# Kernel optimization log

Measured on AMD Instinct MI355X. Metric: run time of the kernel, lower is better.

The kernel has to match this reference:

```python
import math
import jax, jax.numpy as jnp
import numpy as np

TWO_PI = 2.0 * math.pi
LN_EPS = 1e-5


def wrap_angle(a):
    # wrap to (-pi, pi]
    return (a + math.pi) % TWO_PI - math.pi


def setup_inputs() -> dict:
    key = jax.random.key(0)
    ks = jax.random.split(key, 8)
    N = 2000          # num sources / targets (agents)
    E = 200000        # num edges
    D = 4             # input_dim (fixed by RelativeContextPositionEmbedding)
    NF = 64           # num_freq_bands
    H = 128           # hidden_dim
    F = 2 * NF + 1    # fourier feature width per input channel
    source = jax.random.normal(ks[0], (N, 3), jnp.float32)
    target = jax.random.normal(ks[1], (N, 5), jnp.float32)
    edge = jax.random.randint(ks[2], (2, E), 0, N, dtype=jnp.int32)
    freqs = jax.random.normal(ks[3], (D, NF), jnp.float32)          # nn.Embedding(D, NF).weight
    W1 = jax.random.normal(ks[4], (D, F, H), jnp.float32) * 0.02    # per-branch Linear1
    b1 = jnp.zeros((D, H), jnp.float32)
    gamma = jnp.ones((D, H), jnp.float32)                            # per-branch LayerNorm
    beta = jnp.zeros((D, H), jnp.float32)
    W2 = jax.random.normal(ks[5], (D, H, H), jnp.float32) * 0.02    # per-branch Linear2
    b2 = jnp.zeros((D, H), jnp.float32)
    return {"source": source, "target": target, "edge": edge, "freqs": freqs,
            "W1": W1, "b1": b1, "gamma": gamma, "beta": beta, "W2": W2, "b2": b2}


def _compute_feature(source, target, edge):
    src_pos, src_head = source[:, :2], source[:, 2]
    tgt_pos, tgt_head, tgt_speed = target[:, :2], target[:, 2], target[:, 3]
    e0, e1 = edge[0], edge[1]
    pd = src_pos[e0] - tgt_pos[e1]              # [E, 2]
    dx, dy = pd[:, 0], pd[:, 1]
    dh = wrap_angle(src_head[e0] - tgt_head[e1])
    ang = jnp.arctan2(dy, dx)
    tvx = tgt_speed * jnp.cos(tgt_head)
    tvy = tgt_speed * jnp.sin(tgt_head)
    closing = tvx[e1] * jnp.cos(ang) + tvy[e1] * jnp.sin(ang)
    return jnp.stack([dx, dy, dh, closing], axis=-1)  # [E, 4]


def reference(source, target, edge, freqs, W1, b1, gamma, beta, W2, b2):
    # feature computed under torch.no_grad() -> stop_gradient
    feat = jax.lax.stop_gradient(_compute_feature(source, target, edge))  # [E, D]
    x = feat[:, :, None] * freqs[None] * TWO_PI                            # [E, D, NF]
    x = jnp.concatenate([jnp.cos(x), jnp.sin(x), feat[:, :, None]], axis=-1)  # [E, D, F]
    # 4 small Linear -> LayerNorm -> ReLU -> Linear branches, vectorized over D
    h = jnp.einsum('edf,dfh->edh', x, W1) + b1                             # [E, D, H]
    mu = jnp.mean(h, axis=-1, keepdims=True)
    var = jnp.mean(jnp.square(h - mu), axis=-1, keepdims=True)
    h = (h - mu) * jax.lax.rsqrt(var + LN_EPS) * gamma + beta
    h = jax.nn.relu(h)
    y = jnp.einsum('edh,dhk->edk', h, W2) + b2                             # [E, D, H]
    return y.sum(axis=1)                                                   # [E, H]
```

## Files before the change

### kernel.cpp

```cpp
#include <hip/hip_runtime.h>
#include <hip/hip_bf16.h>
#include <math.h>

namespace {

typedef __attribute__((ext_vector_type(8))) short  short8;
typedef __attribute__((ext_vector_type(4))) float  float4v;

constexpr float PI_F     = 3.14159265358979323846f;
constexpr float TWO_PI_F = 6.28318530717958647692f;

__device__ __forceinline__ unsigned pack2(float a, float b) {
    __hip_bfloat162 h = __float22bfloat162_rn(float2{a, b});
    unsigned r;
    __builtin_memcpy(&r, &h, 4);
    return r;
}

union Frag { unsigned u[4]; short8 s; };

__device__ __forceinline__ void gl2lds16(const void* g, void* l) {
    __builtin_amdgcn_global_load_lds(
        (const __attribute__((address_space(1))) void*)g,
        (__attribute__((address_space(3))) void*)l, 16, 0, 0);
}

__device__ __forceinline__ void pb2() {
    asm volatile("s_waitcnt vmcnt(2) lgkmcnt(0)" ::: "memory");
    __builtin_amdgcn_s_barrier();
    __builtin_amdgcn_sched_barrier(0);
}
__device__ __forceinline__ void pb0() {
    asm volatile("s_waitcnt vmcnt(0) lgkmcnt(0)" ::: "memory");
    __builtin_amdgcn_s_barrier();
    __builtin_amdgcn_sched_barrier(0);
}

__global__ __launch_bounds__(256)
void prep_weights(const float* __restrict__ W1,
                  const float* __restrict__ W2,
                  ushort* __restrict__ W1T,
                  ushort* __restrict__ W2T) {
    const int idx = blockIdx.x * 256 + threadIdx.x;
    if (idx < 65536) {
        const int d = idx >> 14;
        const int n = (idx >> 7) & 127;
        const int k = idx & 127;
        __hip_bfloat16 v = __float2bfloat16(W1[(d * 129 + k) * 128 + n]);
        ushort u; __builtin_memcpy(&u, &v, 2);
        W1T[idx] = u;
    } else {
        const int j = idx - 65536;
        const int d = j >> 14;
        const int n = (j >> 7) & 127;
        const int kslot = j & 127;
        const int c = 32 * (kslot >> 5) + 16 * ((kslot >> 2) & 1)
                    + 4 * ((kslot >> 3) & 3) + (kslot & 3);
        __hip_bfloat16 v = __float2bfloat16(W2[(d * 128 + c) * 128 + n]);
        ushort u; __builtin_memcpy(&u, &v, 2);
        W2T[j] = u;
    }
}

__device__ __forceinline__ void stage_half(const ushort* __restrict__ Wtile,
                                           int half, ushort* slot, int wv, int lane) {
    const int e4 = lane & 15;
    const int g  = lane >> 4;
    #pragma unroll
    for (int i = 0; i < 2; ++i) {
        const int c  = 2 * wv + i;
        const int tt = c >> 2;
        const int ks = c & 3;
        const ushort* gp = Wtile + (16 * (4 * half + tt) + e4) * 128 + g * 8 + 32 * ks;
        gl2lds16(gp, slot + c * 512);
    }
}

__global__ __launch_bounds__(512, 4)
void rcpe_rot(const float* __restrict__ source,
              const float* __restrict__ target,
              const int*   __restrict__ edge,
              const float* __restrict__ freqs,
              const float* __restrict__ W1,
              const ushort* __restrict__ W1T,
              const float* __restrict__ b1,
              const float* __restrict__ gamma,
              const float* __restrict__ beta,
              const ushort* __restrict__ W2T,
              const float* __restrict__ b2,
              float* __restrict__ out,
              int E)
{
    __shared__ __align__(16) ushort wbuf[3][8192];
    __shared__ __align__(16) float b1_lds[4][128];
    __shared__ __align__(16) float gm_lds[4][128];
    __shared__ __align__(16) float bt_lds[4][128];
    __shared__ __align__(16) float w1r_lds[4][128];
    __shared__ __align__(16) float feat_lds[4][128];
    __shared__ __align__(16) float freq_lds[4][64];

    const int tid  = threadIdx.x;
    const int wv   = tid >> 6;
    const int lane = tid & 63;
    const int e4   = lane & 15;
    const int g    = lane >> 4;
    const int ebase = blockIdx.x * 128;
    const int eg    = ebase + wv * 16 + e4;

    stage_half(W1T, 0, wbuf[0], wv, lane);
    stage_half(W1T, 1, wbuf[1], wv, lane);
    __builtin_amdgcn_sched_barrier(0);

    {
        const int dd = tid >> 7, c = tid & 127;
        b1_lds[dd][c]  = b1[tid];
        gm_lds[dd][c]  = gamma[tid];
        bt_lds[dd][c]  = beta[tid];
        w1r_lds[dd][c] = W1[(dd * 129 + 128) * 128 + c];
    }
    if (tid < 256) ((float*)freq_lds)[tid] = freqs[tid];

    if (tid < 128) {
        const int e  = ebase + tid;
        const int ec = (e < E) ? e : (E - 1);
        const int s_i = edge[ec];
        const int t_i = edge[E + ec];
        const float sx = source[s_i * 3 + 0];
        const float sy = source[s_i * 3 + 1];
        const float sh = source[s_i * 3 + 2];
        const float tx = target[t_i * 5 + 0];
        const float ty = target[t_i * 5 + 1];
        const float th = target[t_i * 5 + 2];
        const float ts = target[t_i * 5 + 3];
        const float dx = sx - tx;
        const float dy = sy - ty;
        float a = sh - th + PI_F;
        a = fmodf(a, TWO_PI_F);
        if (a < 0.0f) a += TWO_PI_F;
        const float dh  = a - PI_F;
        const float ang = atan2f(dy, dx);
        const float tvx = ts * cosf(th);
        const float tvy = ts * sinf(th);
        const float closing = tvx * cosf(ang) + tvy * sinf(ang);
        feat_lds[0][tid] = dx;
        feat_lds[1][tid] = dy;
        feat_lds[2][tid] = dh;
        feat_lds[3][tid] = closing;
    }

    float4v y[8];
    #pragma unroll
    for (int t = 0; t < 8; ++t) {
        float4v a = {0.f, 0.f, 0.f, 0.f};
        #pragma unroll
        for (int d = 0; d < 4; ++d) {
            const float4v bv = *(const float4v*)(b2 + d * 128 + 16 * t + 4 * g);
            #pragma unroll
            for (int r = 0; r < 4; ++r) a[r] += bv[r];
        }
        y[t] = a;
    }

    pb2();

    ushort* su  = wbuf[0];
    ushort* s1a = wbuf[1];
    ushort* s2a = wbuf[2];
    #define ROTATE() { ushort* _t = su; su = s1a; s1a = s2a; s2a = _t; }

    #pragma unroll 1
    for (int d = 0; d < 4; ++d) {
        const float fe = feat_lds[d][wv * 16 + e4];

        stage_half(W2T + d * 16384, 0, s2a, wv, lane);

        Frag xf[4];
        {
            float cl[8], sl[8], ch8[8], sh8[8];
            #pragma unroll
            for (int j = 0; j < 8; ++j) {
                const float frL = freq_lds[d][8 * g + j];
                const float frH = freq_lds[d][32 + 8 * g + j];
                const float tL = __builtin_amdgcn_fractf(fe * frL);
                const float tH = __builtin_amdgcn_fractf(fe * frH);
                sl[j]  = __builtin_amdgcn_sinf(tL);
                cl[j]  = __builtin_amdgcn_cosf(tL);
                sh8[j] = __builtin_amdgcn_sinf(tH);
                ch8[j] = __builtin_amdgcn_cosf(tH);
            }
            #pragma unroll
            for (int p = 0; p < 4; ++p) {
                xf[0].u[p] = pack2(cl[2 * p],  cl[2 * p + 1]);
                xf[1].u[p] = pack2(ch8[2 * p], ch8[2 * p + 1]);
                xf[2].u[p] = pack2(sl[2 * p],  sl[2 * p + 1]);
                xf[3].u[p] = pack2(sh8[2 * p], sh8[2 * p + 1]);
            }
        }

        float4v hacc[8];
        __builtin_amdgcn_s_setprio(1);
        #pragma unroll
        for (int t = 0; t < 4; ++t) {
            float4v acc = *(const float4v*)&b1_lds[d][16 * t + 4 * g];
            #pragma unroll
            for (int ks = 0; ks < 4; ++ks) {
                const short8 aw = *(const short8*)&su[(t * 4 + ks) * 512 + lane * 8];
                acc = __builtin_amdgcn_mfma_f32_16x16x32_bf16(aw, xf[ks].s, acc, 0, 0, 0);
            }
            hacc[t] = acc;
        }
        __builtin_amdgcn_s_setprio(0);
        pb2();
        ROTATE();

        stage_half(W2T + d * 16384, 1, s2a, wv, lane);

        __builtin_amdgcn_s_setprio(1);
        #pragma unroll
        for (int t = 4; t < 8; ++t) {
            float4v acc = *(const float4v*)&b1_lds[d][16 * t + 4 * g];
            #pragma unroll
            for (int ks = 0; ks < 4; ++ks) {
                const short8 aw = *(const short8*)&su[((t - 4) * 4 + ks) * 512 + lane * 8];
                acc = __builtin_amdgcn_mfma_f32_16x16x32_bf16(aw, xf[ks].s, acc, 0, 0, 0);
            }
            hacc[t] = acc;
        }
        __builtin_amdgcn_s_setprio(0);

        #pragma unroll
        for (int t = 0; t < 8; ++t) {
            const float4v wv4 = *(const float4v*)&w1r_lds[d][16 * t + 4 * g];
            #pragma unroll
            for (int r = 0; r < 4; ++r)
                hacc[t][r] = fmaf(fe, wv4[r], hacc[t][r]);
        }
        pb2();
        ROTATE();

        if (d < 3) stage_half(W1T + (d + 1) * 16384, 0, s2a, wv, lane);

        float sm = 0.f, sq = 0.f;
        #pragma unroll
        for (int t = 0; t < 8; ++t) {
            #pragma unroll
            for (int r = 0; r < 4; ++r) {
                const float v = hacc[t][r];
                sm += v;
                sq = fmaf(v, v, sq);
            }
        }
        sm += __shfl_xor(sm, 16, 64);
        sq += __shfl_xor(sq, 16, 64);
        sm += __shfl_xor(sm, 32, 64);
        sq += __shfl_xor(sq, 32, 64);
        const float mu   = sm * (1.f / 128.f);
        const float var  = sq * (1.f / 128.f) - mu * mu;
        const float rinv = rsqrtf(var + 1e-5f);
        #pragma unroll
        for (int t = 0; t < 8; ++t) {
            const float4v gv = *(const float4v*)&gm_lds[d][16 * t + 4 * g];
            const float4v bv = *(const float4v*)&bt_lds[d][16 * t + 4 * g];
            #pragma unroll
            for (int r = 0; r < 4; ++r) {
                float v = (hacc[t][r] - mu) * rinv;
                v = fmaf(v, gv[r], bv[r]);
                hacc[t][r] = fmaxf(v, 0.f);
            }
        }

        Frag bfr[4];
        #pragma unroll
        for (int ks = 0; ks < 4; ++ks) {
            bfr[ks].u[0] = pack2(hacc[2 * ks][0],     hacc[2 * ks][1]);
            bfr[ks].u[1] = pack2(hacc[2 * ks][2],     hacc[2 * ks][3]);
            bfr[ks].u[2] = pack2(hacc[2 * ks + 1][0], hacc[2 * ks + 1][1]);
            bfr[ks].u[3] = pack2(hacc[2 * ks + 1][2], hacc[2 * ks + 1][3]);
        }

        __builtin_amdgcn_s_setprio(1);
        #pragma unroll
        for (int t = 0; t < 4; ++t) {
            float4v acc = y[t];
            #pragma unroll
            for (int ks = 0; ks < 4; ++ks) {
                const short8 aw = *(const short8*)&su[(t * 4 + ks) * 512 + lane * 8];
                acc = __builtin_amdgcn_mfma_f32_16x16x32_bf16(aw, bfr[ks].s, acc, 0, 0, 0);
            }
            y[t] = acc;
        }
        __builtin_amdgcn_s_setprio(0);
        if (d < 3) pb2(); else pb0();
        ROTATE();

        if (d < 3) stage_half(W1T + (d + 1) * 16384, 1, s2a, wv, lane);

        __builtin_amdgcn_s_setprio(1);
        #pragma unroll
        for (int t = 4; t < 8; ++t) {
            float4v acc = y[t];
            #pragma unroll
            for (int ks = 0; ks < 4; ++ks) {
                const short8 aw = *(const short8*)&su[((t - 4) * 4 + ks) * 512 + lane * 8];
                acc = __builtin_amdgcn_mfma_f32_16x16x32_bf16(aw, bfr[ks].s, acc, 0, 0, 0);
            }
            y[t] = acc;
        }
        __builtin_amdgcn_s_setprio(0);
        if (d < 3) pb2();
        ROTATE();
    }
    #undef ROTATE

    if (eg < E) {
        #pragma unroll
        for (int t = 0; t < 8; ++t) {
            *(float4v*)(out + eg * 128 + 16 * t + 4 * g) = y[t];
        }
    }
}

}

extern "C" void kernel_launch(void* const* d_in, const int* in_sizes, int n_in,
                              void* d_out, int out_size, void* d_ws, size_t ws_size,
                              hipStream_t stream) {
    const float* source = (const float*)d_in[0];
    const float* target = (const float*)d_in[1];
    const int*   edge   = (const int*)  d_in[2];
    const float* freqs  = (const float*)d_in[3];
    const float* W1     = (const float*)d_in[4];
    const float* b1     = (const float*)d_in[5];
    const float* gammap = (const float*)d_in[6];
    const float* betap  = (const float*)d_in[7];
    const float* W2     = (const float*)d_in[8];
    const float* b2     = (const float*)d_in[9];
    float* out = (float*)d_out;

    ushort* W1T = (ushort*)d_ws;
    ushort* W2T = (ushort*)((char*)d_ws + 131072);

    const int E = in_sizes[2] / 2;

    prep_weights<<<dim3(512), dim3(256), 0, stream>>>(W1, W2, W1T, W2T);

    const int nblocks = (E + 127) / 128;
    rcpe_rot<<<dim3(nblocks), dim3(512), 0, stream>>>(
        source, target, edge, freqs, W1, W1T, b1, gammap, betap, W2T, b2, out, E);
}
```

Before: 111.8 us.

## Switch to 32x32x16 MFMA with 4 waves of 32 edges each

```diff
diff --git a/kernel.cpp b/kernel.cpp
--- a/kernel.cpp
+++ b/kernel.cpp
@@ -4,8 +4,10 @@
 
 namespace {
 
-typedef __attribute__((ext_vector_type(8))) short  short8;
-typedef __attribute__((ext_vector_type(4))) float  float4v;
+typedef __attribute__((ext_vector_type(8)))  short    short8;
+typedef __attribute__((ext_vector_type(4)))  float    float4v;
+typedef __attribute__((ext_vector_type(16))) float    f32x16;
+typedef __attribute__((ext_vector_type(4)))  unsigned uint4v;
 
 constexpr float PI_F     = 3.14159265358979323846f;
 constexpr float TWO_PI_F = 6.28318530717958647692f;
@@ -25,8 +27,8 @@
         (__attribute__((address_space(3))) void*)l, 16, 0, 0);
 }
 
-__device__ __forceinline__ void pb2() {
-    asm volatile("s_waitcnt vmcnt(2) lgkmcnt(0)" ::: "memory");
+__device__ __forceinline__ void pb4() {
+    asm volatile("s_waitcnt vmcnt(4) lgkmcnt(0)" ::: "memory");
     __builtin_amdgcn_s_barrier();
     __builtin_amdgcn_sched_barrier(0);
 }
@@ -42,42 +44,42 @@
                   ushort* __restrict__ W1T,
                   ushort* __restrict__ W2T) {
     const int idx = blockIdx.x * 256 + threadIdx.x;
+    const int r   = idx & 0xFFFF;
+    const int d   = r >> 14;
+    const int rem = r & 16383;
+    const int c   = rem >> 9;
+    const int l   = (rem >> 3) & 63;
+    const int j   = rem & 7;
+    const int tau = c >> 3;
+    const int K   = c & 7;
     if (idx < 65536) {
-        const int d = idx >> 14;
-        const int n = (idx >> 7) & 127;
-        const int k = idx & 127;
-        __hip_bfloat16 v = __float2bfloat16(W1[(d * 129 + k) * 128 + n]);
+        const int ch = 32 * tau + (l & 31);
+        const int k  = 16 * K + 8 * (l >> 5) + j;
+        __hip_bfloat16 v = __float2bfloat16(W1[(d * 129 + k) * 128 + ch]);
         ushort u; __builtin_memcpy(&u, &v, 2);
-        W1T[idx] = u;
+        W1T[r] = u;
     } else {
-        const int j = idx - 65536;
-        const int d = j >> 14;
-        const int n = (j >> 7) & 127;
-        const int kslot = j & 127;
-        const int c = 32 * (kslot >> 5) + 16 * ((kslot >> 2) & 1)
-                    + 4 * ((kslot >> 3) & 3) + (kslot & 3);
-        __hip_bfloat16 v = __float2bfloat16(W2[(d * 128 + c) * 128 + n]);
+        const int reg  = 8 * (K & 1) + j;
+        const int ch_h = 32 * (K >> 1) + (reg & 3) + 8 * (reg >> 2) + 4 * (l >> 5);
+        const int chp  = 32 * tau + (l & 31);
+        __hip_bfloat16 v = __float2bfloat16(W2[(d * 128 + ch_h) * 128 + chp]);
         ushort u; __builtin_memcpy(&u, &v, 2);
-        W2T[j] = u;
+        W2T[r] = u;
     }
 }
 
 __device__ __forceinline__ void stage_half(const ushort* __restrict__ Wtile,
                                            int half, ushort* slot, int wv, int lane) {
-    const int e4 = lane & 15;
-    const int g  = lane >> 4;
     #pragma unroll
-    for (int i = 0; i < 2; ++i) {
-        const int c  = 2 * wv + i;
-        const int tt = c >> 2;
-        const int ks = c & 3;
-        const ushort* gp = Wtile + (16 * (4 * half + tt) + e4) * 128 + g * 8 + 32 * ks;
-        gl2lds16(gp, slot + c * 512);
-    }
-}
-
-__global__ __launch_bounds__(512, 4)
-void rcpe_rot(const float* __restrict__ source,
+    for (int i = 0; i < 4; ++i) {
+        const int cl = 4 * wv + i;
+        const int c  = 16 * half + cl;
+        gl2lds16(Wtile + c * 512 + lane * 8, slot + cl * 512);
+    }
+}
+
+__global__ __launch_bounds__(256, 2)
+void rcpe_w32(const float* __restrict__ source,
               const float* __restrict__ target,
               const int*   __restrict__ edge,
               const float* __restrict__ freqs,
@@ -93,32 +95,32 @@
 {
     __shared__ __align__(16) ushort wbuf[3][8192];
     __shared__ __align__(16) float b1_lds[4][128];
-    __shared__ __align__(16) float gm_lds[4][128];
-    __shared__ __align__(16) float bt_lds[4][128];
     __shared__ __align__(16) float w1r_lds[4][128];
+    __shared__ __align__(16) unsigned gmbt_lds[4][128];
     __shared__ __align__(16) float feat_lds[4][128];
     __shared__ __align__(16) float freq_lds[4][64];
 
     const int tid  = threadIdx.x;
     const int wv   = tid >> 6;
     const int lane = tid & 63;
-    const int e4   = lane & 15;
-    const int g    = lane >> 4;
+    const int e5   = lane & 31;
+    const int sh1  = lane >> 5;
     const int ebase = blockIdx.x * 128;
-    const int eg    = ebase + wv * 16 + e4;
+    const int eg    = ebase + wv * 32 + e5;
 
     stage_half(W1T, 0, wbuf[0], wv, lane);
     stage_half(W1T, 1, wbuf[1], wv, lane);
     __builtin_amdgcn_sched_barrier(0);
 
-    {
-        const int dd = tid >> 7, c = tid & 127;
-        b1_lds[dd][c]  = b1[tid];
-        gm_lds[dd][c]  = gamma[tid];
-        bt_lds[dd][c]  = beta[tid];
-        w1r_lds[dd][c] = W1[(dd * 129 + 128) * 128 + c];
-    }
-    if (tid < 256) ((float*)freq_lds)[tid] = freqs[tid];
+    #pragma unroll
+    for (int i = 0; i < 2; ++i) {
+        const int idx = tid + 256 * i;
+        const int dd = idx >> 7, c = idx & 127;
+        b1_lds[dd][c]   = b1[idx];
+        w1r_lds[dd][c]  = W1[(dd * 129 + 128) * 128 + c];
+        gmbt_lds[dd][c] = pack2(gamma[idx], beta[idx]);
+    }
+    ((float*)freq_lds)[tid] = freqs[tid];
 
     if (tid < 128) {
         const int e  = ebase + tid;
@@ -148,20 +150,24 @@
         feat_lds[3][tid] = closing;
     }
 
-    float4v y[8];
+    f32x16 y[4];
     #pragma unroll
-    for (int t = 0; t < 8; ++t) {
-        float4v a = {0.f, 0.f, 0.f, 0.f};
-        #pragma unroll
-        for (int d = 0; d < 4; ++d) {
-            const float4v bv = *(const float4v*)(b2 + d * 128 + 16 * t + 4 * g);
-            #pragma unroll
-            for (int r = 0; r < 4; ++r) a[r] += bv[r];
-        }
-        y[t] = a;
-    }
-
-    pb2();
+    for (int tp = 0; tp < 4; ++tp) {
+        #pragma unroll
+        for (int rq = 0; rq < 4; ++rq) {
+            float4v a = {0.f, 0.f, 0.f, 0.f};
+            #pragma unroll
+            for (int d = 0; d < 4; ++d) {
+                const float4v bv = *(const float4v*)(b2 + d * 128 + 32 * tp + 8 * rq + 4 * sh1);
+                #pragma unroll
+                for (int rr = 0; rr < 4; ++rr) a[rr] += bv[rr];
+            }
+            #pragma unroll
+            for (int rr = 0; rr < 4; ++rr) y[tp][4 * rq + rr] = a[rr];
+        }
+    }
+
+    pb4();
 
     ushort* su  = wbuf[0];
     ushort* s1a = wbuf[1];
@@ -170,152 +176,169 @@
 
     #pragma unroll 1
     for (int d = 0; d < 4; ++d) {
-        const float fe = feat_lds[d][wv * 16 + e4];
-
         stage_half(W2T + d * 16384, 0, s2a, wv, lane);
 
-        Frag xf[4];
-        {
-            float cl[8], sl[8], ch8[8], sh8[8];
+        const float fe = feat_lds[d][wv * 32 + e5];
+
+        Frag xf[8];
+        #pragma unroll
+        for (int K = 0; K < 4; ++K) {
+            float cs[8], sn[8];
             #pragma unroll
             for (int j = 0; j < 8; ++j) {
-                const float frL = freq_lds[d][8 * g + j];
-                const float frH = freq_lds[d][32 + 8 * g + j];
-                const float tL = __builtin_amdgcn_fractf(fe * frL);
-                const float tH = __builtin_amdgcn_fractf(fe * frH);
-                sl[j]  = __builtin_amdgcn_sinf(tL);
-                cl[j]  = __builtin_amdgcn_cosf(tL);
-                sh8[j] = __builtin_amdgcn_sinf(tH);
-                ch8[j] = __builtin_amdgcn_cosf(tH);
-            }
-            #pragma unroll
-            for (int p = 0; p < 4; ++p) {
-                xf[0].u[p] = pack2(cl[2 * p],  cl[2 * p + 1]);
-                xf[1].u[p] = pack2(ch8[2 * p], ch8[2 * p + 1]);
-                xf[2].u[p] = pack2(sl[2 * p],  sl[2 * p + 1]);
-                xf[3].u[p] = pack2(sh8[2 * p], sh8[2 * p + 1]);
-            }
-        }
-
-        float4v hacc[8];
+                const float a = fe * freq_lds[d][16 * K + 8 * sh1 + j];
+                sn[j] = __builtin_amdgcn_sinf(a);
+                cs[j] = __builtin_amdgcn_cosf(a);
+            }
+            #pragma unroll
+            for (int q = 0; q < 4; ++q) {
+                xf[K].u[q]     = pack2(cs[2 * q], cs[2 * q + 1]);
+                xf[K + 4].u[q] = pack2(sn[2 * q], sn[2 * q + 1]);
+            }
+        }
+
+        f32x16 hacc[4];
+        #pragma unroll
+        for (int tp = 0; tp < 2; ++tp) {
+            #pragma unroll
+            for (int rq = 0; rq < 4; ++rq) {
+                const float4v bq = *(const float4v*)&b1_lds[d][32 * tp + 8 * rq + 4 * sh1];
+                const float4v wq = *(const float4v*)&w1r_lds[d][32 * tp + 8 * rq + 4 * sh1];
+                #pragma unroll
+                for (int rr = 0; rr < 4; ++rr)
+                    hacc[tp][4 * rq + rr] = fmaf(fe, wq[rr], bq[rr]);
+            }
+        }
         __builtin_amdgcn_s_setprio(1);
         #pragma unroll
-        for (int t = 0; t < 4; ++t) {
-            float4v acc = *(const float4v*)&b1_lds[d][16 * t + 4 * g];
-            #pragma unroll
-            for (int ks = 0; ks < 4; ++ks) {
-                const short8 aw = *(const short8*)&su[(t * 4 + ks) * 512 + lane * 8];
-                acc = __builtin_amdgcn_mfma_f32_16x16x32_bf16(aw, xf[ks].s, acc, 0, 0, 0);
-            }
-            hacc[t] = acc;
+        for (int K = 0; K < 8; ++K) {
+            #pragma unroll
+            for (int tp = 0; tp < 2; ++tp) {
+                const short8 aw = *(const short8*)&su[(tp * 8 + K) * 512 + lane * 8];
+                hacc[tp] = __builtin_amdgcn_mfma_f32_32x32x16_bf16(aw, xf[K].s, hacc[tp], 0, 0, 0);
+            }
         }
         __builtin_amdgcn_s_setprio(0);
-        pb2();
+        pb4();
         ROTATE();
 
         stage_half(W2T + d * 16384, 1, s2a, wv, lane);
 
+        #pragma unroll
+        for (int tp = 2; tp < 4; ++tp) {
+            #pragma unroll
+            for (int rq = 0; rq < 4; ++rq) {
+                const float4v bq = *(const float4v*)&b1_lds[d][32 * tp + 8 * rq + 4 * sh1];
+                const float4v wq = *(const float4v*)&w1r_lds[d][32 * tp + 8 * rq + 4 * sh1];
+                #pragma unroll
+                for (int rr = 0; rr < 4; ++rr)
+                    hacc[tp][4 * rq + rr] = fmaf(fe, wq[rr], bq[rr]);
+            }
+        }
         __builtin_amdgcn_s_setprio(1);
         #pragma unroll
-        for (int t = 4; t < 8; ++t) {
-            float4v acc = *(const float4v*)&b1_lds[d][16 * t + 4 * g];
-            #pragma unroll
-            for (int ks = 0; ks < 4; ++ks) {
-                const short8 aw = *(const short8*)&su[((t - 4) * 4 + ks) * 512 + lane * 8];
-                acc = __builtin_amdgcn_mfma_f32_16x16x32_bf16(aw, xf[ks].s, acc, 0, 0, 0);
-            }
-            hacc[t] = acc;
+        for (int K = 0; K < 8; ++K) {
+            #pragma unroll
+            for (int tp = 2; tp < 4; ++tp) {
+                const short8 aw = *(const short8*)&su[((tp - 2) * 8 + K) * 512 + lane * 8];
+                hacc[tp] = __builtin_amdgcn_mfma_f32_32x32x16_bf16(aw, xf[K].s, hacc[tp], 0, 0, 0);
+            }
         }
         __builtin_amdgcn_s_setprio(0);
-
-        #pragma unroll
-        for (int t = 0; t < 8; ++t) {
-            const float4v wv4 = *(const float4v*)&w1r_lds[d][16 * t + 4 * g];
-            #pragma unroll
-            for (int r = 0; r < 4; ++r)
-                hacc[t][r] = fmaf(fe, wv4[r], hacc[t][r]);
-        }
-        pb2();
+        pb4();
         ROTATE();
 
         if (d < 3) stage_half(W1T + (d + 1) * 16384, 0, s2a, wv, lane);
 
-        float sm = 0.f, sq = 0.f;
-        #pragma unroll
-        for (int t = 0; t < 8; ++t) {
-            #pragma unroll
-            for (int r = 0; r < 4; ++r) {
-                const float v = hacc[t][r];
-                sm += v;
-                sq = fmaf(v, v, sq);
-            }
-        }
-        sm += __shfl_xor(sm, 16, 64);
-        sq += __shfl_xor(sq, 16, 64);
+        float ps0 = 0.f, ps1 = 0.f, ps2 = 0.f, ps3 = 0.f;
+        float pq0 = 0.f, pq1 = 0.f, pq2 = 0.f, pq3 = 0.f;
+        #pragma unroll
+        for (int tp = 0; tp < 4; ++tp) {
+            #pragma unroll
+            for (int e = 0; e < 4; ++e) {
+                const float v0 = hacc[tp][4 * e + 0];
+                const float v1 = hacc[tp][4 * e + 1];
+                const float v2 = hacc[tp][4 * e + 2];
+                const float v3 = hacc[tp][4 * e + 3];
+                ps0 += v0; pq0 = fmaf(v0, v0, pq0);
+                ps1 += v1; pq1 = fmaf(v1, v1, pq1);
+                ps2 += v2; pq2 = fmaf(v2, v2, pq2);
+                ps3 += v3; pq3 = fmaf(v3, v3, pq3);
+            }
+        }
+        float sm = (ps0 + ps1) + (ps2 + ps3);
+        float sq = (pq0 + pq1) + (pq2 + pq3);
         sm += __shfl_xor(sm, 32, 64);
         sq += __shfl_xor(sq, 32, 64);
         const float mu   = sm * (1.f / 128.f);
         const float var  = sq * (1.f / 128.f) - mu * mu;
         const float rinv = rsqrtf(var + 1e-5f);
         #pragma unroll
-        for (int t = 0; t < 8; ++t) {
-            const float4v gv = *(const float4v*)&gm_lds[d][16 * t + 4 * g];
-            const float4v bv = *(const float4v*)&bt_lds[d][16 * t + 4 * g];
-            #pragma unroll
-            for (int r = 0; r < 4; ++r) {
-                float v = (hacc[t][r] - mu) * rinv;
-                v = fmaf(v, gv[r], bv[r]);
-                hacc[t][r] = fmaxf(v, 0.f);
-            }
-        }
-
-        Frag bfr[4];
-        #pragma unroll
-        for (int ks = 0; ks < 4; ++ks) {
-            bfr[ks].u[0] = pack2(hacc[2 * ks][0],     hacc[2 * ks][1]);
-            bfr[ks].u[1] = pack2(hacc[2 * ks][2],     hacc[2 * ks][3]);
-            bfr[ks].u[2] = pack2(hacc[2 * ks + 1][0], hacc[2 * ks + 1][1]);
-            bfr[ks].u[3] = pack2(hacc[2 * ks + 1][2], hacc[2 * ks + 1][3]);
+        for (int tp = 0; tp < 4; ++tp) {
+            #pragma unroll
+            for (int rq = 0; rq < 4; ++rq) {
+                const uint4v gb = *(const uint4v*)&gmbt_lds[d][32 * tp + 8 * rq + 4 * sh1];
+                #pragma unroll
+                for (int rr = 0; rr < 4; ++rr) {
+                    const float gv = __uint_as_float(gb[rr] << 16);
+                    const float bv = __uint_as_float(gb[rr] & 0xFFFF0000u);
+                    float v = (hacc[tp][4 * rq + rr] - mu) * rinv;
+                    v = fmaf(v, gv, bv);
+                    hacc[tp][4 * rq + rr] = fmaxf(v, 0.f);
+                }
+            }
+        }
+
+        Frag bfr[8];
+        #pragma unroll
+        for (int K = 0; K < 8; ++K) {
+            const int th = K >> 1;
+            const int p  = (K & 1) * 8;
+            #pragma unroll
+            for (int q = 0; q < 4; ++q)
+                bfr[K].u[q] = pack2(hacc[th][p + 2 * q], hacc[th][p + 2 * q + 1]);
         }
 
         __builtin_amdgcn_s_setprio(1);
         #pragma unroll
-        for (int t = 0; t < 4; ++t) {
-            float4v acc = y[t];
-            #pragma unroll
-            for (int ks = 0; ks < 4; ++ks) {
-                const short8 aw = *(const short8*)&su[(t * 4 + ks) * 512 + lane * 8];
-                acc = __builtin_amdgcn_mfma_f32_16x16x32_bf16(aw, bfr[ks].s, acc, 0, 0, 0);
-            }
-            y[t] = acc;
+        for (int K = 0; K < 8; ++K) {
+            #pragma unroll
+            for (int tp = 0; tp < 2; ++tp) {
+                const short8 aw = *(const short8*)&su[(tp * 8 + K) * 512 + lane * 8];
+                y[tp] = __builtin_amdgcn_mfma_f32_32x32x16_bf16(aw, bfr[K].s, y[tp], 0, 0, 0);
+            }
         }
         __builtin_amdgcn_s_setprio(0);
-        if (d < 3) pb2(); else pb0();
+        if (d < 3) pb4(); else pb0();
         ROTATE();
 
         if (d < 3) stage_half(W1T + (d + 1) * 16384, 1, s2a, wv, lane);
 
         __builtin_amdgcn_s_setprio(1);
         #pragma unroll
-        for (int t = 4; t < 8; ++t) {
-            float4v acc = y[t];
-            #pragma unroll
-            for (int ks = 0; ks < 4; ++ks) {
-                const short8 aw = *(const short8*)&su[((t - 4) * 4 + ks) * 512 + lane * 8];
-                acc = __builtin_amdgcn_mfma_f32_16x16x32_bf16(aw, bfr[ks].s, acc, 0, 0, 0);
-            }
-            y[t] = acc;
+        for (int K = 0; K < 8; ++K) {
+            #pragma unroll
+            for (int tp = 2; tp < 4; ++tp) {
+                const short8 aw = *(const short8*)&su[((tp - 2) * 8 + K) * 512 + lane * 8];
+                y[tp] = __builtin_amdgcn_mfma_f32_32x32x16_bf16(aw, bfr[K].s, y[tp], 0, 0, 0);
+            }
         }
         __builtin_amdgcn_s_setprio(0);
-        if (d < 3) pb2();
+        if (d < 3) pb4();
         ROTATE();
     }
     #undef ROTATE
 
     if (eg < E) {
         #pragma unroll
-        for (int t = 0; t < 8; ++t) {
-            *(float4v*)(out + eg * 128 + 16 * t + 4 * g) = y[t];
+        for (int tp = 0; tp < 4; ++tp) {
+            #pragma unroll
+            for (int rq = 0; rq < 4; ++rq) {
+                float4v o;
+                #pragma unroll
+                for (int rr = 0; rr < 4; ++rr) o[rr] = y[tp][4 * rq + rr];
+                *(float4v*)(out + eg * 128 + 32 * tp + 8 * rq + 4 * sh1) = o;
+            }
         }
     }
 }
@@ -345,6 +368,6 @@
     prep_weights<<<dim3(512), dim3(256), 0, stream>>>(W1, W2, W1T, W2T);
 
     const int nblocks = (E + 127) / 128;
-    rcpe_rot<<<dim3(nblocks), dim3(512), 0, stream>>>(
+    rcpe_w32<<<dim3(nblocks), dim3(256), 0, stream>>>(
         source, target, edge, freqs, W1, W1T, b1, gammap, betap, W2T, b2, out, E);
 }
```

After: 116.5 us. 1.04x slower.
